# Kernel optimization log

Hardware: AMD Instinct MI355X
Metric: run time of the kernel (lower is better)

## Reference

```python
import jax, jax.numpy as jnp
import numpy as np

B, T, D_IN, D, N = 8, 1024, 512, 512, 64

def setup_inputs() -> dict:
    key = jax.random.key(0)
    ks = jax.random.split(key, 8)
    s = 0.02  # weight init scale keeps tanh/softmax in sane range
    return {
        'x': jax.random.normal(ks[0], (B, T, D_IN), jnp.float32),
        'h_tape_init': jax.random.normal(ks[1], (B, N, D), jnp.float32),
        'h_work_init': jax.random.normal(ks[2], (B, D), jnp.float32) * 0.1,
        'W_h': jax.random.normal(ks[3], (D, D), jnp.float32) * s,
        'W_xz': jax.random.normal(ks[4], (2 * D, D_IN), jnp.float32) * s,
        'b_h': jnp.zeros((D,), jnp.float32),
        'W_write': jax.random.normal(ks[5], (D, D), jnp.float32) * s,
        'g_z': jnp.ones((D,), jnp.float32),
        'g_r': jnp.ones((D,), jnp.float32),
        'g_h': jnp.ones((D,), jnp.float32),
        'b_gate': jnp.zeros((D,), jnp.float32),
    }

def reference(x, h_tape_init, h_work_init, W_h, W_xz, b_h, W_write, g_z, g_r, g_h, b_gate):
    d = W_h.shape[0]
    scale = 1.0 / np.sqrt(d).astype(np.float32)
    xz = jnp.einsum('btk,ek->bte', x, W_xz)          # [B,T,2D]
    x_proj = xz[..., :d]
    z = xz[..., d:]

    def step(carry, inp):
        h_tape, h_work = carry                        # [B,N,D], [B,D]
        x_t, z_t = inp                                # [B,D], [B,D]
        read_scores = jnp.einsum('bd,bnd->bn', h_work, h_tape) * scale
        read_attn = jax.nn.softmax(read_scores, axis=-1)
        read_val = jnp.einsum('bn,bnd->bd', read_attn, h_tape)
        h_new = jnp.tanh(x_t + h_work @ W_h.T + read_val + b_h)
        write_val = h_new @ W_write.T
        write_scores = jnp.einsum('bd,bnd->bn', write_val, h_tape) * scale
        write_attn = jax.nn.softmax(write_scores, axis=-1)[..., None]  # [B,N,1]
        h_tape_new = h_tape * (1.0 - write_attn) + write_val[:, None, :] * write_attn
        gate_in = jnp.clip(z_t * g_z + read_val * g_r + h_new * g_h + b_gate, -20.0, 20.0)
        out = h_new * jax.nn.silu(gate_in)
        return (h_tape_new, h_new), out

    (h_tape_final, _), outs = jax.lax.scan(
        step, (h_tape_init, h_work_init),
        (jnp.swapaxes(x_proj, 0, 1), jnp.swapaxes(z, 0, 1)))
    return jnp.swapaxes(outs, 0, 1), h_tape_final
```

## Files before the change

kernel.cpp:

```cpp
#include <hip/hip_runtime.h>
#include <math.h>

#define TT 1024
#define DD 512

typedef unsigned int u32;
typedef unsigned long long u64;
typedef _Float16 half2_t __attribute__((ext_vector_type(2)));

static __device__ __forceinline__ u64 aload64(const u64* p) {
    return __hip_atomic_load(p, __ATOMIC_RELAXED, __HIP_MEMORY_SCOPE_AGENT);
}
static __device__ __forceinline__ void astore64(u64* p, u64 v) {
    __hip_atomic_store(p, v, __ATOMIC_RELAXED, __HIP_MEMORY_SCOPE_AGENT);
}
static __device__ __forceinline__ u32 pkh2(float lo, float hi) {
    return __builtin_bit_cast(u32, __builtin_amdgcn_cvt_pkrtz(lo, hi));
}
static __device__ __forceinline__ float2 uph2(u32 v) {
    half2_t h = __builtin_bit_cast(half2_t, v);
    return make_float2((float)h.x, (float)h.y);
}
static __device__ __forceinline__ u64 mkword(u32 pay, u32 tag) {
    return ((u64)tag << 32) | (u64)pay;
}

static __device__ __forceinline__ float redux8(float v) {
    v += __shfl_xor(v, 1); v += __shfl_xor(v, 2); v += __shfl_xor(v, 4); return v;
}
static __device__ __forceinline__ float sum64(float v) {
    #pragma unroll
    for (int o = 32; o > 0; o >>= 1) v += __shfl_xor(v, o);
    return v;
}
static __device__ __forceinline__ float expc(float x) { return __expf(fminf(x, 60.f)); }
static __device__ __forceinline__ float fast_tanh(float x) {
    float xc = fminf(fmaxf(x, -15.f), 15.f);
    float e = __expf(2.f * xc);
    return (e - 1.f) / (e + 1.f);
}

static __device__ __forceinline__ float dot64(const float4 (&w)[16], const float* hr) {
    float a0 = 0.f, a1 = 0.f, a2 = 0.f, a3 = 0.f;
    #pragma unroll
    for (int j = 0; j < 16; j += 4) {
        float4 h0 = *(const float4*)(hr + 4 * (j + 0));
        float4 h1 = *(const float4*)(hr + 4 * (j + 1));
        float4 h2 = *(const float4*)(hr + 4 * (j + 2));
        float4 h3 = *(const float4*)(hr + 4 * (j + 3));
        a0 += w[j + 0].x * h0.x + w[j + 0].y * h0.y + w[j + 0].z * h0.z + w[j + 0].w * h0.w;
        a1 += w[j + 1].x * h1.x + w[j + 1].y * h1.y + w[j + 1].z * h1.z + w[j + 1].w * h1.w;
        a2 += w[j + 2].x * h2.x + w[j + 2].y * h2.y + w[j + 2].z * h2.z + w[j + 2].w * h2.w;
        a3 += w[j + 3].x * h3.x + w[j + 3].y * h3.y + w[j + 3].z * h3.z + w[j + 3].w * h3.w;
    }
    return (a0 + a1) + (a2 + a3);
}

__global__ __launch_bounds__(256) void proj_kernel(const float* __restrict__ x,
                                                   const float* __restrict__ Wxz,
                                                   float* __restrict__ xp,
                                                   float* __restrict__ z) {
    __shared__ float As[16][66];
    __shared__ float Bs[16][66];
    const int m0 = blockIdx.x * 64;
    const int n0 = blockIdx.y * 64;
    const int tid = threadIdx.x;
    const int tm = tid / 16, tn = tid % 16;
    float c[4][4] = {};
    for (int k0 = 0; k0 < 512; k0 += 16) {
        const int r = tid >> 2, c4 = (tid & 3) * 4;
        float4 a4 = *(const float4*)(x + (size_t)(m0 + r) * 512 + k0 + c4);
        float4 b4 = *(const float4*)(Wxz + (size_t)(n0 + r) * 512 + k0 + c4);
        As[c4 + 0][r] = a4.x; As[c4 + 1][r] = a4.y; As[c4 + 2][r] = a4.z; As[c4 + 3][r] = a4.w;
        Bs[c4 + 0][r] = b4.x; Bs[c4 + 1][r] = b4.y; Bs[c4 + 2][r] = b4.z; Bs[c4 + 3][r] = b4.w;
        __syncthreads();
        #pragma unroll
        for (int k = 0; k < 16; ++k) {
            float a0 = As[k][tm * 4 + 0], a1 = As[k][tm * 4 + 1];
            float a2 = As[k][tm * 4 + 2], a3 = As[k][tm * 4 + 3];
            float b0 = Bs[k][tn * 4 + 0], b1 = Bs[k][tn * 4 + 1];
            float b2 = Bs[k][tn * 4 + 2], b3 = Bs[k][tn * 4 + 3];
            c[0][0] += a0 * b0; c[0][1] += a0 * b1; c[0][2] += a0 * b2; c[0][3] += a0 * b3;
            c[1][0] += a1 * b0; c[1][1] += a1 * b1; c[1][2] += a1 * b2; c[1][3] += a1 * b3;
            c[2][0] += a2 * b0; c[2][1] += a2 * b1; c[2][2] += a2 * b2; c[2][3] += a2 * b3;
            c[3][0] += a3 * b0; c[3][1] += a3 * b1; c[3][2] += a3 * b2; c[3][3] += a3 * b3;
        }
        __syncthreads();
    }
    #pragma unroll
    for (int i = 0; i < 4; ++i) {
        const int m = m0 + tm * 4 + i;
        #pragma unroll
        for (int j = 0; j < 4; ++j) {
            const int e = n0 + tn * 4 + j;
            if (e < 512) xp[(size_t)m * 512 + e] = c[i][j];
            else         z[(size_t)m * 512 + (e - 512)] = c[i][j];
        }
    }
}

__global__ __launch_bounds__(512) void rec_kernel(
    const float* __restrict__ tape0, const float* __restrict__ hwork0,
    const float* __restrict__ W_h, const float* __restrict__ b_h,
    const float* __restrict__ W_write,
    const float* __restrict__ g_z, const float* __restrict__ g_r,
    const float* __restrict__ g_h, const float* __restrict__ b_gate,
    const float* __restrict__ Zbuf,
    float* __restrict__ out, float* __restrict__ tape_out,
    u64* hA, u64* cA, u64* bB, u64* hB) {
    __shared__ float tpd[64][65];
    __shared__ float hw2[8][68];
    __shared__ float red[8][64];
    __shared__ float2 bred[8][64];
    __shared__ float2 cred[8][32];
    __shared__ float wvc[64], rvc[64], hhc[64], hnc[64], xpc[64], zc[64], a_l[64], c1_l[64];
    __shared__ float hwv_s[8];
    __shared__ float c2_s;

    const int b = blockIdx.x & 7, s = blockIdx.x >> 3;
    const int tid = threadIdx.x, lane = tid & 63, wid = tid >> 6;
    const int n8 = tid >> 3, l = tid & 7;
    const int d0 = s * 64;
    const float scale = 0.044194173824159216f;

    float4 wh[16];
    float4 wwc[16];
    {
        const float4* w1 = (const float4*)(W_h + (size_t)(d0 + n8) * DD + l * 64);
        #pragma unroll
        for (int j = 0; j < 16; ++j) wh[j] = w1[j];
        const float4* w2 = (const float4*)(W_write + (size_t)tid * DD + d0);
        #pragma unroll
        for (int j = 0; j < 16; ++j) wwc[j] = w2[j];
    }
    float bhr = 0.f, gz = 0.f, gr = 0.f, gh = 0.f, bg = 0.f;
    if (wid == 0) bhr = b_h[d0 + lane];
    if (wid == 1) { gz = g_z[d0 + lane]; gr = g_r[d0 + lane]; gh = g_h[d0 + lane]; bg = b_gate[d0 + lane]; }

    {
        const int n = tid >> 3, c0 = (tid & 7) * 8;
        const float* src = tape0 + ((size_t)(b * 64 + n)) * DD + d0 + c0;
        #pragma unroll
        for (int i = 0; i < 8; ++i) tpd[n][c0 + i] = src[i];
    }
    hw2[tid >> 6][tid & 63] = hwork0[(size_t)b * DD + tid];
    if (tid < 64) { wvc[tid] = 0.f; a_l[tid] = 0.f; }
    if (tid == 0) c2_s = 0.f;
    __syncthreads();

    {
        float pq = 0.f;
        #pragma unroll
        for (int i = 0; i < 8; ++i) pq += hw2[s][l * 8 + i] * tpd[n8][l * 8 + i];
        pq = redux8(pq);
        if (l == 0)
            astore64(&bB[(((size_t)1 * 8 + b) * 8 + s) * 64 + n8], mkword(pkh2(0.f, pq), 0u));
    }
    {
        const int n = tid & 63, j = tid >> 6;
        const u64* p = &bB[(((size_t)1 * 8 + b) * 8 + j) * 64 + n];
        u64 v;
        for (;;) { v = aload64(p); if ((u32)(v >> 32) == 0u) break; __builtin_amdgcn_s_sleep(1); }
        bred[j][n] = uph2((u32)v);
    }
    __syncthreads();
    if (wid == 0) {
        float q0 = 0.f;
        #pragma unroll
        for (int j = 0; j < 8; ++j) q0 += bred[j][lane].y;
        float er = expc(scale * q0);
        float Zr = sum64(er);
        c1_l[lane] = __fdividef(er, Zr);
    }
    __syncthreads();

    for (int t = 0; t < TT; ++t) {
        const int pA = t & 1, pB = t & 1;
        const u32 tg = (u32)(t + 1);

        float xpr = 0.f, zr = 0.f;
        if (wid == 2)      xpr = out[((size_t)(b * TT + t)) * DD + d0 + lane];
        else if (wid == 3) zr  = Zbuf[((size_t)(b * TT + t)) * DD + d0 + lane];

        {
            float acc = dot64(wh, &hw2[l][0]);
            acc = redux8(acc);
            if (l == 0) hhc[n8] = acc;
        }
        {
            float acc = 0.f;
            const float wvd = wvc[lane];
            #pragma unroll
            for (int k = 0; k < 8; ++k) {
                const int n = wid * 8 + k;
                float tp = tpd[n][lane];
                acc += c1_l[n] * tp;
                tpd[n][lane] = tp + a_l[n] * (wvd - tp);
            }
            red[wid][lane] = acc;
        }
        if (wid == 2)      xpc[lane] = xpr;
        else if (wid == 3) zc[lane] = zr;
        __syncthreads();
        if (wid == 0) {
            float acc = c2_s * wvc[lane];
            #pragma unroll
            for (int g = 0; g < 8; ++g) acc += red[g][lane];
            rvc[lane] = acc;
            hnc[lane] = fast_tanh(xpc[lane] + hhc[lane] + acc + bhr);
        }
        __syncthreads();
        if (wid == 1) {
            float h = hnc[lane];
            float g = zc[lane] * gz + rvc[lane] * gr + h * gh + bg;
            g = fminf(fmaxf(g, -20.f), 20.f);
            float sig = 1.f / (1.f + __expf(-g));
            out[((size_t)(b * TT + t)) * DD + d0 + lane] = h * g * sig;
        }
        if (wid == 0 && (lane & 1) == 0)
            astore64(&hA[((size_t)pA * 8 + b) * 256 + s * 32 + (lane >> 1)],
                     mkword(pkh2(hnc[lane], hnc[lane + 1]), tg));
        {
            float cj = 0.f;
            #pragma unroll
            for (int j = 0; j < 16; ++j) {
                float4 h4 = *(const float4*)&hnc[4 * j];
                cj += wwc[j].x * h4.x + wwc[j].y * h4.y + wwc[j].z * h4.z + wwc[j].w * h4.w;
            }
            float cn = __shfl_xor(cj, 1);
            if ((tid & 1) == 0)
                astore64(&cA[(((size_t)pA * 8 + b) * 8 + s) * 256 + (tid >> 1)],
                         mkword(pkh2(cj, cn), tg));
        }
        if (tid < 256) {
            const u64* p = &hA[((size_t)pA * 8 + b) * 256 + tid];
            u64 v;
            for (;;) { v = aload64(p); if ((u32)(v >> 32) == tg) break; __builtin_amdgcn_s_sleep(1); }
            float2 hp = uph2((u32)v);
            hw2[tid >> 5][2 * (tid & 31)] = hp.x;
            hw2[tid >> 5][2 * (tid & 31) + 1] = hp.y;
        } else {
            const int k = tid - 256, j = k >> 5, w = k & 31;
            const u64* p = &cA[(((size_t)pA * 8 + b) * 8 + j) * 256 + s * 32 + w];
            u64 v;
            for (;;) { v = aload64(p); if ((u32)(v >> 32) == tg) break; __builtin_amdgcn_s_sleep(1); }
            cred[j][w] = uph2((u32)v);
        }
        __syncthreads();
        if (wid == 0 && lane < 32) {
            float lo = 0.f, hi = 0.f;
            #pragma unroll
            for (int j = 0; j < 8; ++j) { float2 c = cred[j][lane]; lo += c.x; hi += c.y; }
            wvc[2 * lane] = lo; wvc[2 * lane + 1] = hi;
        }
        __syncthreads();
        {
            float pw = 0.f, pq = 0.f;
            #pragma unroll
            for (int i = 0; i < 8; ++i) {
                float tp = tpd[n8][l * 8 + i];
                pw += wvc[l * 8 + i] * tp;
                pq += hnc[l * 8 + i] * tp;
            }
            pw = redux8(pw); pq = redux8(pq);
            if (l == 0)
                astore64(&bB[(((size_t)pB * 8 + b) * 8 + s) * 64 + n8],
                         mkword(pkh2(pw, pq), tg));
        }
        if (wid == 1) {
            float hv = sum64(hnc[lane] * wvc[lane]);
            if (lane == 0) astore64(&hB[((size_t)pB * 8 + b) * 8 + s], mkword(pkh2(hv, 0.f), tg));
        }
        {
            const int n = tid & 63, j = tid >> 6;
            const u64* p = &bB[(((size_t)pB * 8 + b) * 8 + j) * 64 + n];
            u64 v;
            for (;;) { v = aload64(p); if ((u32)(v >> 32) == tg) break; __builtin_amdgcn_s_sleep(1); }
            bred[j][n] = uph2((u32)v);
        }
        if (tid < 8) {
            const u64* p = &hB[((size_t)pB * 8 + b) * 8 + tid];
            u64 v;
            for (;;) { v = aload64(p); if ((u32)(v >> 32) == tg) break; __builtin_amdgcn_s_sleep(1); }
            hwv_s[tid] = uph2((u32)v).x;
        }
        __syncthreads();
        if (wid == 0) {
            float ws = 0.f, q0 = 0.f;
            #pragma unroll
            for (int j = 0; j < 8; ++j) { float2 v = bred[j][lane]; ws += v.x; q0 += v.y; }
            float hv = 0.f;
            #pragma unroll
            for (int j = 0; j < 8; ++j) hv += hwv_s[j];
            float ew = expc(scale * ws);
            float Zw = sum64(ew);
            float a = __fdividef(ew, Zw);
            float er = expc(scale * ((1.f - a) * q0 + a * hv));
            float Zr = sum64(er);
            float r = __fdividef(er, Zr);
            a_l[lane] = a;
            c1_l[lane] = r * (1.f - a);
            float c2 = sum64(r * a);
            if (lane == 0) c2_s = c2;
        }
        __syncthreads();
    }

    {
        const int n = tid >> 3, c0 = (tid & 7) * 8;
        const float an = a_l[n];
        float* dst = tape_out + ((size_t)(b * 64 + n)) * DD + d0 + c0;
        #pragma unroll
        for (int i = 0; i < 8; ++i) {
            float tp = tpd[n][c0 + i];
            tp += an * (wvc[c0 + i] - tp);
            dst[i] = tp;
        }
    }
}

extern "C" void kernel_launch(void* const* d_in, const int* in_sizes, int n_in,
                              void* d_out, int out_size, void* d_ws, size_t ws_size,
                              hipStream_t stream) {
    const float* x       = (const float*)d_in[0];
    const float* tape0   = (const float*)d_in[1];
    const float* hwork0  = (const float*)d_in[2];
    const float* W_h     = (const float*)d_in[3];
    const float* W_xz    = (const float*)d_in[4];
    const float* b_h     = (const float*)d_in[5];
    const float* W_write = (const float*)d_in[6];
    const float* g_z     = (const float*)d_in[7];
    const float* g_r     = (const float*)d_in[8];
    const float* g_h     = (const float*)d_in[9];
    const float* b_gate  = (const float*)d_in[10];

    float* out  = (float*)d_out;
    float* tout = out + (size_t)8 * TT * DD;

    char* ws = (char*)d_ws;
    u64* hA   = (u64*)ws;
    u64* cA   = (u64*)(ws + 32768);
    u64* bB   = (u64*)(ws + 294912);
    u64* hB   = (u64*)(ws + 360448);
    float* Zbuf = (float*)(ws + 393216);

    (void)in_sizes; (void)n_in; (void)out_size; (void)ws_size;

    dim3 pgrid(128, 16);
    proj_kernel<<<pgrid, 256, 0, stream>>>(x, W_xz, out, Zbuf);
    rec_kernel<<<64, 512, 0, stream>>>(tape0, hwork0, W_h, b_h, W_write,
                                       g_z, g_r, g_h, b_gate, Zbuf,
                                       out, tout, hA, cA, bB, hB);
}
```

Baseline: 4.932 ms.

## Replicate full tape slice per block to drop second cross-block exchange per step

Each block now keeps the whole 64x512 tape for its batch in shared memory, stored with an XOR swizzle. It computes the write and read scores locally from the full write vector and h_work, so the second per-step global exchange (bB/hB partial dot products) is removed. The cA and hA exchanges are merged into one wait phase, tape updates are split around the atomic loads to hide their latency, and the xp/z loads are prefetched one step ahead. In exchange each block does eight times the tape update and dot-product work, and shared memory use rises to about 128KB.

```diff
diff --git a/kernel.cpp b/kernel.cpp
--- a/kernel.cpp
+++ b/kernel.cpp
@@ -38,22 +38,6 @@
     float xc = fminf(fmaxf(x, -15.f), 15.f);
     float e = __expf(2.f * xc);
     return (e - 1.f) / (e + 1.f);
-}
-
-static __device__ __forceinline__ float dot64(const float4 (&w)[16], const float* hr) {
-    float a0 = 0.f, a1 = 0.f, a2 = 0.f, a3 = 0.f;
-    #pragma unroll
-    for (int j = 0; j < 16; j += 4) {
-        float4 h0 = *(const float4*)(hr + 4 * (j + 0));
-        float4 h1 = *(const float4*)(hr + 4 * (j + 1));
-        float4 h2 = *(const float4*)(hr + 4 * (j + 2));
-        float4 h3 = *(const float4*)(hr + 4 * (j + 3));
-        a0 += w[j + 0].x * h0.x + w[j + 0].y * h0.y + w[j + 0].z * h0.z + w[j + 0].w * h0.w;
-        a1 += w[j + 1].x * h1.x + w[j + 1].y * h1.y + w[j + 1].z * h1.z + w[j + 1].w * h1.w;
-        a2 += w[j + 2].x * h2.x + w[j + 2].y * h2.y + w[j + 2].z * h2.z + w[j + 2].w * h2.w;
-        a3 += w[j + 3].x * h3.x + w[j + 3].y * h3.y + w[j + 3].z * h3.z + w[j + 3].w * h3.w;
-    }
-    return (a0 + a1) + (a2 + a3);
 }
 
 __global__ __launch_bounds__(256) void proj_kernel(const float* __restrict__ x,
@@ -107,26 +91,27 @@
     const float* __restrict__ g_h, const float* __restrict__ b_gate,
     const float* __restrict__ Zbuf,
     float* __restrict__ out, float* __restrict__ tape_out,
-    u64* hA, u64* cA, u64* bB, u64* hB) {
-    __shared__ float tpd[64][65];
-    __shared__ float hw2[8][68];
+    u64* hA, u64* cA) {
+    __shared__ __align__(16) float tp[64][512];
+    __shared__ __align__(16) float hw2[8][68];
+    __shared__ __align__(16) float wvp[8][68];
     __shared__ float red[8][64];
-    __shared__ float2 bred[8][64];
-    __shared__ float2 cred[8][32];
-    __shared__ float wvc[64], rvc[64], hhc[64], hnc[64], xpc[64], zc[64], a_l[64], c1_l[64];
-    __shared__ float hwv_s[8];
+    __shared__ __align__(16) float hnc[64];
+    __shared__ float rvc[64], xpc[64], zc[64];
+    __shared__ float a_l[64], c1_l[64], hhc[64], ws_l[64], q0_l[64];
     __shared__ float c2_s;
 
     const int b = blockIdx.x & 7, s = blockIdx.x >> 3;
     const int tid = threadIdx.x, lane = tid & 63, wid = tid >> 6;
-    const int n8 = tid >> 3, l = tid & 7;
+    const int nrow = tid >> 3, l = tid & 7;
+    const int sw = (nrow & 7) << 2;
     const int d0 = s * 64;
     const float scale = 0.044194173824159216f;
 
     float4 wh[16];
     float4 wwc[16];
     {
-        const float4* w1 = (const float4*)(W_h + (size_t)(d0 + n8) * DD + l * 64);
+        const float4* w1 = (const float4*)(W_h + (size_t)(d0 + nrow) * DD + l * 64);
         #pragma unroll
         for (int j = 0; j < 16; ++j) wh[j] = w1[j];
         const float4* w2 = (const float4*)(W_write + (size_t)tid * DD + d0);
@@ -138,78 +123,82 @@
     if (wid == 1) { gz = g_z[d0 + lane]; gr = g_r[d0 + lane]; gh = g_h[d0 + lane]; bg = b_gate[d0 + lane]; }
 
     {
-        const int n = tid >> 3, c0 = (tid & 7) * 8;
-        const float* src = tape0 + ((size_t)(b * 64 + n)) * DD + d0 + c0;
-        #pragma unroll
-        for (int i = 0; i < 8; ++i) tpd[n][c0 + i] = src[i];
+        const float* src = tape0 + (size_t)(b * 64 + nrow) * DD;
+        #pragma unroll
+        for (int i = 0; i < 16; ++i) {
+            float4 v = *(const float4*)(src + l * 64 + 4 * i);
+            *(float4*)&tp[nrow][(l * 64 + 4 * i) ^ sw] = v;
+        }
     }
     hw2[tid >> 6][tid & 63] = hwork0[(size_t)b * DD + tid];
-    if (tid < 64) { wvc[tid] = 0.f; a_l[tid] = 0.f; }
+    {
+        float* pw = &wvp[0][0];
+        for (int i = tid; i < 8 * 68; i += 512) pw[i] = 0.f;
+    }
+    if (tid < 64) a_l[tid] = 0.f;
     if (tid == 0) c2_s = 0.f;
+    float xpr = 0.f, zr = 0.f;
+    if (wid == 2)      xpr = out[((size_t)(b * TT)) * DD + d0 + lane];
+    else if (wid == 3) zr  = Zbuf[((size_t)(b * TT)) * DD + d0 + lane];
     __syncthreads();
 
     {
-        float pq = 0.f;
-        #pragma unroll
-        for (int i = 0; i < 8; ++i) pq += hw2[s][l * 8 + i] * tpd[n8][l * 8 + i];
-        pq = redux8(pq);
-        if (l == 0)
-            astore64(&bB[(((size_t)1 * 8 + b) * 8 + s) * 64 + n8], mkword(pkh2(0.f, pq), 0u));
-    }
-    {
-        const int n = tid & 63, j = tid >> 6;
-        const u64* p = &bB[(((size_t)1 * 8 + b) * 8 + j) * 64 + n];
-        u64 v;
-        for (;;) { v = aload64(p); if ((u32)(v >> 32) == 0u) break; __builtin_amdgcn_s_sleep(1); }
-        bred[j][n] = uph2((u32)v);
+        float q0 = 0.f, hh = 0.f;
+        #pragma unroll
+        for (int i = 0; i < 16; ++i) {
+            float4 t4 = *(const float4*)&tp[nrow][(l * 64 + 4 * i) ^ sw];
+            float4 h4 = *(const float4*)&hw2[l][4 * i];
+            q0 += t4.x * h4.x + t4.y * h4.y + t4.z * h4.z + t4.w * h4.w;
+            hh += wh[i].x * h4.x + wh[i].y * h4.y + wh[i].z * h4.z + wh[i].w * h4.w;
+        }
+        q0 = redux8(q0); hh = redux8(hh);
+        if (l == 0) { q0_l[nrow] = q0; hhc[nrow] = hh; }
     }
     __syncthreads();
     if (wid == 0) {
-        float q0 = 0.f;
-        #pragma unroll
-        for (int j = 0; j < 8; ++j) q0 += bred[j][lane].y;
-        float er = expc(scale * q0);
+        float er = expc(scale * q0_l[lane]);
         float Zr = sum64(er);
         c1_l[lane] = __fdividef(er, Zr);
     }
     __syncthreads();
 
     for (int t = 0; t < TT; ++t) {
-        const int pA = t & 1, pB = t & 1;
+        const int p = t & 1;
         const u32 tg = (u32)(t + 1);
 
-        float xpr = 0.f, zr = 0.f;
-        if (wid == 2)      xpr = out[((size_t)(b * TT + t)) * DD + d0 + lane];
-        else if (wid == 3) zr  = Zbuf[((size_t)(b * TT + t)) * DD + d0 + lane];
-
-        {
-            float acc = dot64(wh, &hw2[l][0]);
-            acc = redux8(acc);
-            if (l == 0) hhc[n8] = acc;
-        }
+        if (wid == 2)      xpc[lane] = xpr;
+        else if (wid == 3) zc[lane] = zr;
         {
             float acc = 0.f;
-            const float wvd = wvc[lane];
-            #pragma unroll
-            for (int k = 0; k < 8; ++k) {
-                const int n = wid * 8 + k;
-                float tp = tpd[n][lane];
-                acc += c1_l[n] * tp;
-                tpd[n][lane] = tp + a_l[n] * (wvd - tp);
+            #pragma unroll
+            for (int k = 0; k < 8; ++k)
+                acc += c1_l[wid * 8 + k] * tp[wid * 8 + k][(d0 + lane) ^ (k << 2)];
+            red[wid][lane] = acc;
+        }
+        __syncthreads();
+        if (wid == 0) {
+            float rv = c2_s * wvp[s][lane];
+            #pragma unroll
+            for (int w = 0; w < 8; ++w) rv += red[w][lane];
+            rvc[lane] = rv;
+            hnc[lane] = fast_tanh(xpc[lane] + hhc[lane] + rv + bhr);
+        }
+        __syncthreads();
+        if (wid == 0 && !(lane & 1))
+            astore64(&hA[((size_t)p * 8 + b) * 256 + s * 32 + (lane >> 1)],
+                     mkword(pkh2(hnc[lane], hnc[lane + 1]), tg));
+        {
+            float cj = 0.f;
+            #pragma unroll
+            for (int j = 0; j < 16; ++j) {
+                float4 h4 = *(const float4*)&hnc[4 * j];
+                cj += wwc[j].x * h4.x + wwc[j].y * h4.y + wwc[j].z * h4.z + wwc[j].w * h4.w;
             }
-            red[wid][lane] = acc;
-        }
-        if (wid == 2)      xpc[lane] = xpr;
-        else if (wid == 3) zc[lane] = zr;
-        __syncthreads();
-        if (wid == 0) {
-            float acc = c2_s * wvc[lane];
-            #pragma unroll
-            for (int g = 0; g < 8; ++g) acc += red[g][lane];
-            rvc[lane] = acc;
-            hnc[lane] = fast_tanh(xpc[lane] + hhc[lane] + acc + bhr);
-        }
-        __syncthreads();
+            float cn = __shfl_xor(cj, 1);
+            if (!(tid & 1))
+                astore64(&cA[(((size_t)p * 8 + b) * 8 + s) * 256 + (tid >> 1)],
+                         mkword(pkh2(cj, cn), tg));
+        }
         if (wid == 1) {
             float h = hnc[lane];
             float g = zc[lane] * gz + rvc[lane] * gr + h * gh + bg;
@@ -217,85 +206,110 @@
             float sig = 1.f / (1.f + __expf(-g));
             out[((size_t)(b * TT + t)) * DD + d0 + lane] = h * g * sig;
         }
-        if (wid == 0 && (lane & 1) == 0)
-            astore64(&hA[((size_t)pA * 8 + b) * 256 + s * 32 + (lane >> 1)],
-                     mkword(pkh2(hnc[lane], hnc[lane + 1]), tg));
+        const float an = a_l[nrow];
+        #pragma unroll
+        for (int i = 0; i < 8; ++i) {
+            const int c = (l * 64 + 4 * i) ^ sw;
+            float4 t4 = *(const float4*)&tp[nrow][c];
+            float4 w4 = *(const float4*)&wvp[l][4 * i];
+            t4.x += an * (w4.x - t4.x); t4.y += an * (w4.y - t4.y);
+            t4.z += an * (w4.z - t4.z); t4.w += an * (w4.w - t4.w);
+            *(float4*)&tp[nrow][c] = t4;
+        }
+        u64 v0 = 0, v1 = 0, v2 = 0, v3 = 0, v4 = 0, v5 = 0, v6 = 0, v7 = 0, vhw = 0;
+        if (tid < 256) {
+            const u64* cb = cA + (((size_t)p * 8 + b) * 8) * 256 + tid;
+            v0 = aload64(cb + 0 * 256); v1 = aload64(cb + 1 * 256);
+            v2 = aload64(cb + 2 * 256); v3 = aload64(cb + 3 * 256);
+            v4 = aload64(cb + 4 * 256); v5 = aload64(cb + 5 * 256);
+            v6 = aload64(cb + 6 * 256); v7 = aload64(cb + 7 * 256);
+        } else {
+            vhw = aload64(hA + ((size_t)p * 8 + b) * 256 + (tid - 256));
+        }
+        #pragma unroll
+        for (int i = 8; i < 16; ++i) {
+            const int c = (l * 64 + 4 * i) ^ sw;
+            float4 t4 = *(const float4*)&tp[nrow][c];
+            float4 w4 = *(const float4*)&wvp[l][4 * i];
+            t4.x += an * (w4.x - t4.x); t4.y += an * (w4.y - t4.y);
+            t4.z += an * (w4.z - t4.z); t4.w += an * (w4.w - t4.w);
+            *(float4*)&tp[nrow][c] = t4;
+        }
+        __syncthreads();
+        if (tid < 256) {
+            const u64* cb = cA + (((size_t)p * 8 + b) * 8) * 256 + tid;
+            for (;;) {
+                u32 m = 0;
+                if ((u32)(v0 >> 32) == tg) m |= 1u;   if ((u32)(v1 >> 32) == tg) m |= 2u;
+                if ((u32)(v2 >> 32) == tg) m |= 4u;   if ((u32)(v3 >> 32) == tg) m |= 8u;
+                if ((u32)(v4 >> 32) == tg) m |= 16u;  if ((u32)(v5 >> 32) == tg) m |= 32u;
+                if ((u32)(v6 >> 32) == tg) m |= 64u;  if ((u32)(v7 >> 32) == tg) m |= 128u;
+                if (m == 0xffu) break;
+                __builtin_amdgcn_s_sleep(1);
+                if (!(m & 1u))   v0 = aload64(cb + 0 * 256);
+                if (!(m & 2u))   v1 = aload64(cb + 1 * 256);
+                if (!(m & 4u))   v2 = aload64(cb + 2 * 256);
+                if (!(m & 8u))   v3 = aload64(cb + 3 * 256);
+                if (!(m & 16u))  v4 = aload64(cb + 4 * 256);
+                if (!(m & 32u))  v5 = aload64(cb + 5 * 256);
+                if (!(m & 64u))  v6 = aload64(cb + 6 * 256);
+                if (!(m & 128u)) v7 = aload64(cb + 7 * 256);
+            }
+            float lo = 0.f, hi = 0.f; float2 f;
+            f = uph2((u32)v0); lo += f.x; hi += f.y;
+            f = uph2((u32)v1); lo += f.x; hi += f.y;
+            f = uph2((u32)v2); lo += f.x; hi += f.y;
+            f = uph2((u32)v3); lo += f.x; hi += f.y;
+            f = uph2((u32)v4); lo += f.x; hi += f.y;
+            f = uph2((u32)v5); lo += f.x; hi += f.y;
+            f = uph2((u32)v6); lo += f.x; hi += f.y;
+            f = uph2((u32)v7); lo += f.x; hi += f.y;
+            wvp[tid >> 5][2 * (tid & 31)]     = lo;
+            wvp[tid >> 5][2 * (tid & 31) + 1] = hi;
+        } else {
+            const int k = tid - 256;
+            const u64* hb = hA + ((size_t)p * 8 + b) * 256 + k;
+            for (;;) {
+                if ((u32)(vhw >> 32) == tg) break;
+                __builtin_amdgcn_s_sleep(1);
+                vhw = aload64(hb);
+            }
+            float2 hp = uph2((u32)vhw);
+            hw2[k >> 5][2 * (k & 31)]     = hp.x;
+            hw2[k >> 5][2 * (k & 31) + 1] = hp.y;
+        }
+        __syncthreads();
+        float hwv = 0.f;
         {
-            float cj = 0.f;
-            #pragma unroll
-            for (int j = 0; j < 16; ++j) {
-                float4 h4 = *(const float4*)&hnc[4 * j];
-                cj += wwc[j].x * h4.x + wwc[j].y * h4.y + wwc[j].z * h4.z + wwc[j].w * h4.w;
+            float ws = 0.f, q0 = 0.f, hh = 0.f;
+            #pragma unroll
+            for (int i = 0; i < 16; ++i) {
+                float4 t4 = *(const float4*)&tp[nrow][(l * 64 + 4 * i) ^ sw];
+                float4 w4 = *(const float4*)&wvp[l][4 * i];
+                float4 h4 = *(const float4*)&hw2[l][4 * i];
+                ws += w4.x * t4.x + w4.y * t4.y + w4.z * t4.z + w4.w * t4.w;
+                q0 += h4.x * t4.x + h4.y * t4.y + h4.z * t4.z + h4.w * t4.w;
+                hh += wh[i].x * h4.x + wh[i].y * h4.y + wh[i].z * h4.z + wh[i].w * h4.w;
             }
-            float cn = __shfl_xor(cj, 1);
-            if ((tid & 1) == 0)
-                astore64(&cA[(((size_t)pA * 8 + b) * 8 + s) * 256 + (tid >> 1)],
-                         mkword(pkh2(cj, cn), tg));
-        }
-        if (tid < 256) {
-            const u64* p = &hA[((size_t)pA * 8 + b) * 256 + tid];
-            u64 v;
-            for (;;) { v = aload64(p); if ((u32)(v >> 32) == tg) break; __builtin_amdgcn_s_sleep(1); }
-            float2 hp = uph2((u32)v);
-            hw2[tid >> 5][2 * (tid & 31)] = hp.x;
-            hw2[tid >> 5][2 * (tid & 31) + 1] = hp.y;
-        } else {
-            const int k = tid - 256, j = k >> 5, w = k & 31;
-            const u64* p = &cA[(((size_t)pA * 8 + b) * 8 + j) * 256 + s * 32 + w];
-            u64 v;
-            for (;;) { v = aload64(p); if ((u32)(v >> 32) == tg) break; __builtin_amdgcn_s_sleep(1); }
-            cred[j][w] = uph2((u32)v);
-        }
-        __syncthreads();
-        if (wid == 0 && lane < 32) {
-            float lo = 0.f, hi = 0.f;
-            #pragma unroll
-            for (int j = 0; j < 8; ++j) { float2 c = cred[j][lane]; lo += c.x; hi += c.y; }
-            wvc[2 * lane] = lo; wvc[2 * lane + 1] = hi;
-        }
-        __syncthreads();
-        {
-            float pw = 0.f, pq = 0.f;
-            #pragma unroll
-            for (int i = 0; i < 8; ++i) {
-                float tp = tpd[n8][l * 8 + i];
-                pw += wvc[l * 8 + i] * tp;
-                pq += hnc[l * 8 + i] * tp;
-            }
-            pw = redux8(pw); pq = redux8(pq);
-            if (l == 0)
-                astore64(&bB[(((size_t)pB * 8 + b) * 8 + s) * 64 + n8],
-                         mkword(pkh2(pw, pq), tg));
-        }
-        if (wid == 1) {
-            float hv = sum64(hnc[lane] * wvc[lane]);
-            if (lane == 0) astore64(&hB[((size_t)pB * 8 + b) * 8 + s], mkword(pkh2(hv, 0.f), tg));
-        }
-        {
-            const int n = tid & 63, j = tid >> 6;
-            const u64* p = &bB[(((size_t)pB * 8 + b) * 8 + j) * 64 + n];
-            u64 v;
-            for (;;) { v = aload64(p); if ((u32)(v >> 32) == tg) break; __builtin_amdgcn_s_sleep(1); }
-            bred[j][n] = uph2((u32)v);
-        }
-        if (tid < 8) {
-            const u64* p = &hB[((size_t)pB * 8 + b) * 8 + tid];
-            u64 v;
-            for (;;) { v = aload64(p); if ((u32)(v >> 32) == tg) break; __builtin_amdgcn_s_sleep(1); }
-            hwv_s[tid] = uph2((u32)v).x;
-        }
-        __syncthreads();
+            ws = redux8(ws); q0 = redux8(q0); hh = redux8(hh);
+            if (l == 0) { ws_l[nrow] = ws; q0_l[nrow] = q0; hhc[nrow] = hh; }
+        }
         if (wid == 0) {
-            float ws = 0.f, q0 = 0.f;
-            #pragma unroll
-            for (int j = 0; j < 8; ++j) { float2 v = bred[j][lane]; ws += v.x; q0 += v.y; }
-            float hv = 0.f;
-            #pragma unroll
-            for (int j = 0; j < 8; ++j) hv += hwv_s[j];
-            float ew = expc(scale * ws);
+            const int r8 = lane >> 3, c8 = (lane & 7) * 8;
+            float a = 0.f;
+            #pragma unroll
+            for (int k = 0; k < 8; ++k) a += hw2[r8][c8 + k] * wvp[r8][c8 + k];
+            hwv = sum64(a);
+        }
+        if (wid == 2 && t + 1 < TT)      xpr = out[((size_t)(b * TT + t + 1)) * DD + d0 + lane];
+        else if (wid == 3 && t + 1 < TT) zr  = Zbuf[((size_t)(b * TT + t + 1)) * DD + d0 + lane];
+        __syncthreads();
+        if (wid == 0) {
+            float ew = expc(scale * ws_l[lane]);
             float Zw = sum64(ew);
             float a = __fdividef(ew, Zw);
-            float er = expc(scale * ((1.f - a) * q0 + a * hv));
+            float q = (1.f - a) * q0_l[lane] + a * hwv;
+            float er = expc(scale * q);
             float Zr = sum64(er);
             float r = __fdividef(er, Zr);
             a_l[lane] = a;
@@ -307,14 +321,16 @@
     }
 
     {
-        const int n = tid >> 3, c0 = (tid & 7) * 8;
-        const float an = a_l[n];
-        float* dst = tape_out + ((size_t)(b * 64 + n)) * DD + d0 + c0;
-        #pragma unroll
-        for (int i = 0; i < 8; ++i) {
-            float tp = tpd[n][c0 + i];
-            tp += an * (wvc[c0 + i] - tp);
-            dst[i] = tp;
+        const float an = a_l[nrow];
+        float* dst = tape_out + ((size_t)(b * 64 + nrow)) * DD;
+        #pragma unroll
+        for (int i = 0; i < 2; ++i) {
+            const int c0 = d0 + l * 8 + 4 * i;
+            float4 t4 = *(const float4*)&tp[nrow][c0 ^ sw];
+            float4 w4 = *(const float4*)&wvp[s][l * 8 + 4 * i];
+            t4.x += an * (w4.x - t4.x); t4.y += an * (w4.y - t4.y);
+            t4.z += an * (w4.z - t4.z); t4.w += an * (w4.w - t4.w);
+            *(float4*)(dst + c0) = t4;
         }
     }
 }
@@ -340,8 +356,6 @@
     char* ws = (char*)d_ws;
     u64* hA   = (u64*)ws;
     u64* cA   = (u64*)(ws + 32768);
-    u64* bB   = (u64*)(ws + 294912);
-    u64* hB   = (u64*)(ws + 360448);
     float* Zbuf = (float*)(ws + 393216);
 
     (void)in_sizes; (void)n_in; (void)out_size; (void)ws_size;
@@ -350,5 +364,5 @@
     proj_kernel<<<pgrid, 256, 0, stream>>>(x, W_xz, out, Zbuf);
     rec_kernel<<<64, 512, 0, stream>>>(tape0, hwork0, W_h, b_h, W_write,
                                        g_z, g_r, g_h, b_gate, Zbuf,
-                                       out, tout, hA, cA, bB, hB);
-}
+                                       out, tout, hA, cA);
+}
```

New measurement: 8.530 ms. 72.9% more time.
